# Kernel tuning notes

Measured on AMD Instinct MI355X. Metric: run time of the kernel, lower is better.

Reference implementation:

```python
import jax, jax.numpy as jnp
import numpy as np

NEG_SLOPE = 0.2
EPS = 1e-12


def setup_inputs() -> dict:
    key = jax.random.key(0)
    k1, k2, k3, k4, k5 = jax.random.split(key, 5)
    N, E, IN, OUT = 100000, 1600000, 256, 64
    x = jax.random.normal(k1, (N, IN), dtype=jnp.float32)
    edge_index = jax.random.randint(k2, (2, E), 0, N, dtype=jnp.int64)
    # GATConv (heads=1) parameters: lin weight, att_src, att_dst, bias
    W = jax.random.normal(k3, (IN, OUT), dtype=jnp.float32) * (1.0 / np.sqrt(IN))
    att_src = jax.random.normal(k4, (OUT,), dtype=jnp.float32) * (1.0 / np.sqrt(OUT))
    att_dst = jax.random.normal(k5, (OUT,), dtype=jnp.float32) * (1.0 / np.sqrt(OUT))
    bias = jnp.zeros((OUT,), dtype=jnp.float32)
    return {"x": x, "edge_index": edge_index, "W": W,
            "att_src": att_src, "att_dst": att_dst, "bias": bias}


def reference(x, edge_index, W, att_src, att_dst, bias):
    N = x.shape[0]
    # PyG GATConv default add_self_loops=True
    loops = jnp.arange(N, dtype=edge_index.dtype)
    src = jnp.concatenate([edge_index[0], loops])  # source j of edge (j -> i)
    dst = jnp.concatenate([edge_index[1], loops])  # target i (softmax segment)

    h = x @ W                                      # [N, out]
    a_src = h @ att_src                            # [N] per-node source score
    a_dst = h @ att_dst                            # [N] per-node target score

    e = jax.nn.leaky_relu(a_src[src] + a_dst[dst], NEG_SLOPE)  # [E+N]
    # segment softmax over incoming edges of each destination node
    e_max = jax.ops.segment_max(e, dst, num_segments=N)
    e = jnp.exp(e - e_max[dst])
    denom = jax.ops.segment_sum(e, dst, num_segments=N)
    alpha = e / denom[dst]                         # [E+N]

    # scatter-aggregate: out[i] = sum_j alpha_ij * h[j]
    out = jax.ops.segment_sum(alpha[:, None] * h[src], dst, num_segments=N)
    out = out + bias

    # dropout (p=0.3) in eval mode is identity; then F.normalize (row-wise L2)
    nrm = jnp.sqrt(jnp.sum(out * out, axis=-1, keepdims=True))
    return out / jnp.maximum(nrm, EPS)
```

## Files before the change

kernel.cpp:

```cpp
#include <hip/hip_runtime.h>
#include <hip/hip_bf16.h>
#include <math.h>

#define NEG_SLOPE 0.2f
#define EPS_NRM 1e-12f
#define K_IN 256
#define C_OUT 64

typedef __attribute__((ext_vector_type(8))) short bf16x8;
typedef __attribute__((ext_vector_type(4))) float f32x4;

__device__ __forceinline__ unsigned short bf16_rne(float v) {
    unsigned u = __float_as_uint(v);
    return (unsigned short)((u + 0x7fffu + ((u >> 16) & 1u)) >> 16);
}

__global__ __launch_bounds__(256) void wsplit(
    const float* __restrict__ W, unsigned short* __restrict__ Wt_hi,
    unsigned short* __restrict__ Wt_lo)
{
    int tid = blockIdx.x * blockDim.x + threadIdx.x;
    if (tid >= K_IN * C_OUT) return;
    int k = tid >> 6, c = tid & 63;
    float v = W[tid];
    unsigned short hb = bf16_rne(v);
    float vh = __uint_as_float((unsigned)hb << 16);
    unsigned short lb = bf16_rne(v - vh);
    Wt_hi[c * K_IN + k] = hb;
    Wt_lo[c * K_IN + k] = lb;
}

__global__ __launch_bounds__(256) void gemm_att(
    const float* __restrict__ x,
    const unsigned short* __restrict__ Wt_hi,
    const unsigned short* __restrict__ Wt_lo,
    const float* __restrict__ att_s, const float* __restrict__ att_d,
    __hip_bfloat16* __restrict__ h, float* __restrict__ a_src_arr,
    float* __restrict__ a_dst_arr, int N,
    const int* __restrict__ dstA, int* __restrict__ cnt,
    int* __restrict__ rank, int E)
{
    int t      = threadIdx.x;
    int gtid   = blockIdx.x * blockDim.x + t;
    int stride = gridDim.x * blockDim.x;

    int r0 = 0, r1 = 0, r2 = 0, r3 = 0;
    int i0 = gtid, i1 = gtid + stride, i2 = gtid + 2 * stride,
        i3 = gtid + 3 * stride;
    if (i0 < E) r0 = atomicAdd(&cnt[dstA[i0]], 1);
    if (i1 < E) r1 = atomicAdd(&cnt[dstA[i1]], 1);
    if (i2 < E) r2 = atomicAdd(&cnt[dstA[i2]], 1);
    if (i3 < E) r3 = atomicAdd(&cnt[dstA[i3]], 1);
    for (int i = gtid + 4 * stride; i < E; i += stride)
        rank[i] = atomicAdd(&cnt[dstA[i]], 1);

    int gw  = gtid >> 6;
    int l   = t & 63;
    int lm  = l & 15;
    int grp = l >> 4;
    int row0 = gw * 16;

    int srow = row0 + lm; if (srow >= N) srow = N - 1;
    const float* xq = x + (size_t)srow * K_IN + grp * 8;

    const unsigned short* wbh = Wt_hi + (size_t)lm * K_IN + grp * 8;
    const unsigned short* wbl = Wt_lo + (size_t)lm * K_IN + grp * 8;

    f32x4 acc[4];
#pragma unroll
    for (int n = 0; n < 4; ++n) acc[n] = (f32x4){0.f, 0.f, 0.f, 0.f};

    float4 xa = *(const float4*)(xq);
    float4 xb = *(const float4*)(xq + 4);

    for (int kt = 0; kt < K_IN / 32; ++kt) {
        float4 xa2, xb2;
        if (kt < K_IN / 32 - 1) {
            xa2 = *(const float4*)(xq + (kt + 1) * 32);
            xb2 = *(const float4*)(xq + (kt + 1) * 32 + 4);
        }
        short sh[8], sl[8];
        const float* fa = (const float*)&xa;
        const float* fb = (const float*)&xb;
#pragma unroll
        for (int i = 0; i < 4; ++i) {
            float v0 = fa[i], v1 = fb[i];
            unsigned short h0 = bf16_rne(v0), h1 = bf16_rne(v1);
            sh[i] = (short)h0; sh[i + 4] = (short)h1;
            sl[i]     = (short)bf16_rne(v0 - __uint_as_float((unsigned)h0 << 16));
            sl[i + 4] = (short)bf16_rne(v1 - __uint_as_float((unsigned)h1 << 16));
        }
        bf16x8 xh = *(bf16x8*)&sh[0];
        bf16x8 xl = *(bf16x8*)&sl[0];

        int ko = kt * 32;
#pragma unroll
        for (int n = 0; n < 4; ++n) {
            bf16x8 wh = *(const bf16x8*)(wbh + (size_t)n * 16 * K_IN + ko);
            bf16x8 wl = *(const bf16x8*)(wbl + (size_t)n * 16 * K_IN + ko);
            acc[n] = __builtin_amdgcn_mfma_f32_16x16x32_bf16(wh, xh, acc[n], 0, 0, 0);
            acc[n] = __builtin_amdgcn_mfma_f32_16x16x32_bf16(wl, xh, acc[n], 0, 0, 0);
            acc[n] = __builtin_amdgcn_mfma_f32_16x16x32_bf16(wh, xl, acc[n], 0, 0, 0);
        }
        xa = xa2; xb = xb2;
    }

    int row = row0 + lm;
    float ps = 0.f, pd = 0.f;
#pragma unroll
    for (int n = 0; n < 4; ++n) {
        float4 as4 = *(const float4*)(att_s + n * 16 + grp * 4);
        float4 ad4 = *(const float4*)(att_d + n * 16 + grp * 4);
        f32x4 a = acc[n];
        ps += a.x * as4.x + a.y * as4.y + a.z * as4.z + a.w * as4.w;
        pd += a.x * ad4.x + a.y * ad4.y + a.z * ad4.z + a.w * ad4.w;
    }
    ps += __shfl_xor(ps, 16, 64); ps += __shfl_xor(ps, 32, 64);
    pd += __shfl_xor(pd, 16, 64); pd += __shfl_xor(pd, 32, 64);
    if (row < N) {
        if (grp == 0) { a_src_arr[row] = ps; a_dst_arr[row] = pd; }
#pragma unroll
        for (int n = 0; n < 4; ++n) {
            f32x4 a = acc[n];
            __hip_bfloat16 b0 = __float2bfloat16(a.x);
            __hip_bfloat16 b1 = __float2bfloat16(a.y);
            __hip_bfloat16 b2 = __float2bfloat16(a.z);
            __hip_bfloat16 b3 = __float2bfloat16(a.w);
            unsigned long long pk =
                (unsigned long long)*(unsigned short*)&b0 |
                ((unsigned long long)*(unsigned short*)&b1 << 16) |
                ((unsigned long long)*(unsigned short*)&b2 << 32) |
                ((unsigned long long)*(unsigned short*)&b3 << 48);
            *(unsigned long long*)(h + (size_t)row * C_OUT + n * 16 + grp * 4) = pk;
        }
    }

    if (i0 < E) rank[i0] = r0;
    if (i1 < E) rank[i1] = r1;
    if (i2 < E) rank[i2] = r2;
    if (i3 < E) rank[i3] = r3;
}

__global__ __launch_bounds__(256) void scan_p1(
    const int* __restrict__ cnt, int* __restrict__ partials, int n)
{
    int b = blockIdx.x, t = threadIdx.x;
    int base = b * 1024;
    int s = 0;
#pragma unroll
    for (int j = 0; j < 4; ++j) {
        int i = base + t * 4 + j;
        if (i < n) s += cnt[i];
    }
    for (int d = 1; d < 64; d <<= 1) s += __shfl_xor(s, d, 64);
    __shared__ int wsum[4];
    int lane = t & 63, wid = t >> 6;
    if (lane == 0) wsum[wid] = s;
    __syncthreads();
    if (t == 0) partials[b] = wsum[0] + wsum[1] + wsum[2] + wsum[3];
}

__global__ __launch_bounds__(256) void scan_p2(int* partials, int nb)
{
    __shared__ int buf[256];
    int t = threadIdx.x;
    int v = (t < nb) ? partials[t] : 0;
    buf[t] = v;
    __syncthreads();
    for (int d = 1; d < 256; d <<= 1) {
        int w = (t >= d) ? buf[t - d] : 0;
        __syncthreads();
        buf[t] += w;
        __syncthreads();
    }
    if (t < nb) partials[t] = buf[t] - v;
}

__global__ __launch_bounds__(256) void scan_p3(
    const int* __restrict__ cnt, const int* __restrict__ partials,
    int* __restrict__ offsets, int n)
{
    int b = blockIdx.x, t = threadIdx.x;
    int base = b * 1024;
    int v[4];
    int s = 0;
#pragma unroll
    for (int j = 0; j < 4; ++j) {
        int i = base + t * 4 + j;
        v[j] = (i < n) ? cnt[i] : 0;
        s += v[j];
    }
    int lane = t & 63, wid = t >> 6;
    int incl = s;
    for (int d = 1; d < 64; d <<= 1) {
        int w = __shfl_up(incl, d, 64);
        if (lane >= d) incl += w;
    }
    __shared__ int wsum[4];
    __shared__ int wbase[4];
    if (lane == 63) wsum[wid] = incl;
    __syncthreads();
    if (t == 0) {
        int r = 0;
        for (int i = 0; i < 4; ++i) { wbase[i] = r; r += wsum[i]; }
    }
    __syncthreads();
    int run = partials[b] + wbase[wid] + (incl - s);
#pragma unroll
    for (int j = 0; j < 4; ++j) {
        int i = base + t * 4 + j;
        if (i < n) {
            offsets[i] = run;
            run += v[j];
            if (i == n - 1) offsets[n] = run;
        }
    }
}

__global__ __launch_bounds__(256) void scatter_edges(
    const int* __restrict__ srcA, const int* __restrict__ dstA,
    const int* __restrict__ offsets, const int* __restrict__ rank,
    const float* __restrict__ a_src, const float* __restrict__ a_dst,
    unsigned long long* __restrict__ csr, int E)
{
    int i = blockIdx.x * blockDim.x + threadIdx.x;
    if (i >= E) return;
    int s = srcA[i], d = dstA[i];
    float e = a_src[s] + a_dst[d];
    e = fmaxf(e, NEG_SLOPE * e);
    float w = __expf(e);
    int pos = offsets[d] + rank[i];
    unsigned long long packed =
        (unsigned long long)(unsigned)s |
        ((unsigned long long)__float_as_uint(w) << 32);
    __builtin_nontemporal_store(packed, &csr[pos]);
}

__global__ __launch_bounds__(256) void gat_pull(
    const int* __restrict__ offsets, const int2* __restrict__ csr,
    const unsigned short* __restrict__ h, const float* __restrict__ a_src,
    const float* __restrict__ a_dst, const float* __restrict__ bias,
    float* __restrict__ out, int N)
{
    int gw   = (blockIdx.x * blockDim.x + threadIdx.x) >> 6;
    int lane = threadIdx.x & 63;
    int grp  = lane >> 4;
    int gl   = lane & 15;
    int node = gw * 4 + grp;
    bool valid = node < N;
    int nv = valid ? node : 0;

    int beg = offsets[nv];
    int n   = valid ? (offsets[nv + 1] - beg) : 0;
    const int2* ce = csr + (n ? beg : 0);

    float asv = a_src[nv], adv = a_dst[nv];
    float es = asv + adv; es = fmaxf(es, NEG_SLOPE * es);
    float ws = __expf(es);
    unsigned long long hu = *(const unsigned long long*)
        (h + (size_t)nv * C_OUT + 4 * gl);
    unsigned hl = (unsigned)hu, hh = (unsigned)(hu >> 32);
    float acc0 = ws * __uint_as_float(hl << 16);
    float acc1 = ws * __uint_as_float(hl & 0xffff0000u);
    float acc2 = ws * __uint_as_float(hh << 16);
    float acc3 = ws * __uint_as_float(hh & 0xffff0000u);
    float den = ws;

    int2 c0 = ce[0];
    int2 c1 = ce[(n > 1) ? 1 : 0];
    unsigned long long u0 = *(const unsigned long long*)
        (h + (size_t)c0.x * C_OUT + 4 * gl);
    unsigned long long u1 = *(const unsigned long long*)
        (h + (size_t)c1.x * C_OUT + 4 * gl);

    for (int p = 0; p < n; p += 2) {
        int2 m0 = ce[(p + 2 < n) ? p + 2 : 0];
        int2 m1 = ce[(p + 3 < n) ? p + 3 : 0];
        unsigned long long v0 = *(const unsigned long long*)
            (h + (size_t)m0.x * C_OUT + 4 * gl);
        unsigned long long v1 = *(const unsigned long long*)
            (h + (size_t)m1.x * C_OUT + 4 * gl);

        float w0 = __int_as_float(c0.y);
        float w1 = (p + 1 < n) ? __int_as_float(c1.y) : 0.f;
        unsigned l0 = (unsigned)u0, h0 = (unsigned)(u0 >> 32);
        unsigned l1 = (unsigned)u1, h1 = (unsigned)(u1 >> 32);
        den  += w0 + w1;
        acc0 += w0 * __uint_as_float(l0 << 16)
              + w1 * __uint_as_float(l1 << 16);
        acc1 += w0 * __uint_as_float(l0 & 0xffff0000u)
              + w1 * __uint_as_float(l1 & 0xffff0000u);
        acc2 += w0 * __uint_as_float(h0 << 16)
              + w1 * __uint_as_float(h1 << 16);
        acc3 += w0 * __uint_as_float(h0 & 0xffff0000u)
              + w1 * __uint_as_float(h1 & 0xffff0000u);

        c0 = m0; c1 = m1; u0 = v0; u1 = v1;
    }

    float4 bl = *(const float4*)(bias + 4 * gl);
    float rd = 1.f / den;
    float o0 = acc0 * rd + bl.x;
    float o1 = acc1 * rd + bl.y;
    float o2 = acc2 * rd + bl.z;
    float o3 = acc3 * rd + bl.w;

    float sq = o0 * o0 + o1 * o1 + o2 * o2 + o3 * o3;
#pragma unroll
    for (int d = 1; d < 16; d <<= 1) sq += __shfl_xor(sq, d, 64);
    float rn = 1.f / fmaxf(sqrtf(sq), EPS_NRM);

    if (valid)
        *(float4*)(out + (size_t)node * C_OUT + 4 * gl) =
            make_float4(o0 * rn, o1 * rn, o2 * rn, o3 * rn);
}

extern "C" void kernel_launch(void* const* d_in, const int* in_sizes, int n_in,
                              void* d_out, int out_size, void* d_ws, size_t ws_size,
                              hipStream_t stream)
{
    const float* x     = (const float*)d_in[0];
    const int*   ei    = (const int*)d_in[1];
    const float* W     = (const float*)d_in[2];
    const float* att_s = (const float*)d_in[3];
    const float* att_d = (const float*)d_in[4];
    const float* bias  = (const float*)d_in[5];
    float*       out   = (float*)d_out;

    const int OUT = in_sizes[3];
    const int IN  = in_sizes[2] / OUT;
    const int N   = in_sizes[0] / IN;
    const int E   = in_sizes[1] / 2;

    char* w = (char*)d_ws;
    auto alloc = [&](size_t bytes) -> void* {
        void* p = (void*)w;
        w += (bytes + 255) & ~(size_t)255;
        return p;
    };
    __hip_bfloat16* h = (__hip_bfloat16*)alloc((size_t)N * C_OUT * 2);
    float* a_src  = (float*)alloc((size_t)N * 4);
    float* a_dst  = (float*)alloc((size_t)N * 4);
    int*   cnt    = (int*)alloc((size_t)N * 4);
    int*   offs   = (int*)alloc((size_t)(N + 1) * 4);
    int*   parts  = (int*)alloc(1024 * 4);
    unsigned short* Wt_hi = (unsigned short*)alloc((size_t)K_IN * C_OUT * 2);
    unsigned short* Wt_lo = (unsigned short*)alloc((size_t)K_IN * C_OUT * 2);
    int*   rank   = (int*)alloc((size_t)E * 4);
    unsigned long long* csr = (unsigned long long*)alloc((size_t)E * 8);

    hipMemsetAsync(cnt, 0, (size_t)N * 4, stream);

    wsplit<<<(K_IN * C_OUT + 255) / 256, 256, 0, stream>>>(W, Wt_hi, Wt_lo);

    gemm_att<<<(N + 63) / 64, 256, 0, stream>>>(
        x, Wt_hi, Wt_lo, att_s, att_d, h, a_src, a_dst, N, ei + E, cnt,
        rank, E);

    int NB = (N + 1023) / 1024;
    scan_p1<<<NB, 256, 0, stream>>>(cnt, parts, N);
    scan_p2<<<1, 256, 0, stream>>>(parts, NB);
    scan_p3<<<NB, 256, 0, stream>>>(cnt, parts, offs, N);

    scatter_edges<<<(E + 255) / 256, 256, 0, stream>>>(
        ei, ei + E, offs, rank, a_src, a_dst, csr, E);

    gat_pull<<<(N + 15) / 16, 256, 0, stream>>>(offs, (const int2*)csr,
        (const unsigned short*)h, a_src, a_dst, bias, out, N);
}
```

Before: 374.0 us.

## Split edge histogram into dedicated blocks within the GEMM launch

Before, every GEMM thread also did a grid-strided share of the destination-count atomics, so each thread took histogram latency before its matrix work. Now the launch adds 256 extra blocks that do only the atomic histogram and rank writes, with four loads batched per thread, and the GEMM blocks do only the projection. This lets the two kinds of work run concurrently on separate waves instead of being serialized inside each thread. The risk is load imbalance: 256 blocks handling 1.6M atomics may finish after the GEMM blocks and become the critical path.

After: 372.0 us. Within noise of the previous version (-0.5%).

```diff
diff --git a/kernel.cpp b/kernel.cpp
--- a/kernel.cpp
+++ b/kernel.cpp
@@ -6,6 +6,7 @@
 #define EPS_NRM 1e-12f
 #define K_IN 256
 #define C_OUT 64
+#define HIST_BLOCKS 256
 
 typedef __attribute__((ext_vector_type(8))) short bf16x8;
 typedef __attribute__((ext_vector_type(4))) float f32x4;
@@ -38,23 +39,32 @@
     __hip_bfloat16* __restrict__ h, float* __restrict__ a_src_arr,
     float* __restrict__ a_dst_arr, int N,
     const int* __restrict__ dstA, int* __restrict__ cnt,
-    int* __restrict__ rank, int E)
-{
-    int t      = threadIdx.x;
-    int gtid   = blockIdx.x * blockDim.x + t;
-    int stride = gridDim.x * blockDim.x;
-
-    int r0 = 0, r1 = 0, r2 = 0, r3 = 0;
-    int i0 = gtid, i1 = gtid + stride, i2 = gtid + 2 * stride,
-        i3 = gtid + 3 * stride;
-    if (i0 < E) r0 = atomicAdd(&cnt[dstA[i0]], 1);
-    if (i1 < E) r1 = atomicAdd(&cnt[dstA[i1]], 1);
-    if (i2 < E) r2 = atomicAdd(&cnt[dstA[i2]], 1);
-    if (i3 < E) r3 = atomicAdd(&cnt[dstA[i3]], 1);
-    for (int i = gtid + 4 * stride; i < E; i += stride)
-        rank[i] = atomicAdd(&cnt[dstA[i]], 1);
-
-    int gw  = gtid >> 6;
+    int* __restrict__ rank, int E, int GB)
+{
+    int t = threadIdx.x;
+
+    if (blockIdx.x >= GB) {
+        int tid  = (blockIdx.x - GB) * 256 + t;
+        int step = HIST_BLOCKS * 256;
+        for (int i = tid; i < E; i += 4 * step) {
+            int j1 = i + step, j2 = i + 2 * step, j3 = i + 3 * step;
+            int d0 = dstA[i];
+            int d1 = (j1 < E) ? dstA[j1] : 0;
+            int d2 = (j2 < E) ? dstA[j2] : 0;
+            int d3 = (j3 < E) ? dstA[j3] : 0;
+            int r0 = atomicAdd(&cnt[d0], 1);
+            int r1 = (j1 < E) ? atomicAdd(&cnt[d1], 1) : 0;
+            int r2 = (j2 < E) ? atomicAdd(&cnt[d2], 1) : 0;
+            int r3 = (j3 < E) ? atomicAdd(&cnt[d3], 1) : 0;
+            rank[i] = r0;
+            if (j1 < E) rank[j1] = r1;
+            if (j2 < E) rank[j2] = r2;
+            if (j3 < E) rank[j3] = r3;
+        }
+        return;
+    }
+
+    int gw  = blockIdx.x * 4 + (t >> 6);
     int l   = t & 63;
     int lm  = l & 15;
     int grp = l >> 4;
@@ -134,11 +144,6 @@
             *(unsigned long long*)(h + (size_t)row * C_OUT + n * 16 + grp * 4) = pk;
         }
     }
-
-    if (i0 < E) rank[i0] = r0;
-    if (i1 < E) rank[i1] = r1;
-    if (i2 < E) rank[i2] = r2;
-    if (i3 < E) rank[i3] = r3;
 }
 
 __global__ __launch_bounds__(256) void scan_p1(
@@ -353,9 +358,10 @@
 
     wsplit<<<(K_IN * C_OUT + 255) / 256, 256, 0, stream>>>(W, Wt_hi, Wt_lo);
 
-    gemm_att<<<(N + 63) / 64, 256, 0, stream>>>(
+    int GB = (N + 63) / 64;
+    gemm_att<<<GB + HIST_BLOCKS, 256, 0, stream>>>(
         x, Wt_hi, Wt_lo, att_s, att_d, h, a_src, a_dst, N, ei + E, cnt,
-        rank, E);
+        rank, E, GB);
 
     int NB = (N + 1023) / 1024;
     scan_p1<<<NB, 256, 0, stream>>>(cnt, parts, N);
```
